# Optimization experiments

Hardware: AMD Instinct MI355X
Metric: run time of the kernel (lower is better)

Reference implementation:

```python
import jax, jax.numpy as jnp
import numpy as np

SEQ_LEN = 128
EMBED_DIM = 1024
BATCH = 128


def setup_inputs() -> dict:
    key = jax.random.key(0)
    ks = jax.random.split(key, 9)
    d = EMBED_DIM
    s = 0.02
    return {
        "x": jax.random.normal(ks[0], (BATCH, SEQ_LEN * d), dtype=jnp.float32),
        "Wq": jax.random.normal(ks[1], (d, d), dtype=jnp.float32) * s,
        "bq": jax.random.normal(ks[2], (d,), dtype=jnp.float32) * s,
        "Wk": jax.random.normal(ks[3], (d, d), dtype=jnp.float32) * s,
        "bk": jax.random.normal(ks[4], (d,), dtype=jnp.float32) * s,
        "Wv": jax.random.normal(ks[5], (d, d), dtype=jnp.float32) * s,
        "bv": jax.random.normal(ks[6], (d,), dtype=jnp.float32) * s,
        "Wo": jax.random.normal(ks[7], (d, d), dtype=jnp.float32) * s,
        "bo": jax.random.normal(ks[8], (d,), dtype=jnp.float32) * s,
    }


def reference(x, Wq, bq, Wk, bk, Wv, bv, Wo, bo):
    b = x.shape[0]
    d = EMBED_DIM
    xs = x.reshape(b, SEQ_LEN, d)  # [B, S, D]
    # torch Linear: y = x @ W.T + b
    Q = jnp.einsum("bsd,ed->bse", xs, Wq) + bq
    K = jnp.einsum("bsd,ed->bse", xs, Wk) + bk
    V = jnp.einsum("bsd,ed->bse", xs, Wv) + bv
    scores = jnp.einsum("bse,bte->bst", Q, K) / jnp.sqrt(jnp.float32(d))
    weights = jax.nn.softmax(scores, axis=-1)
    attended = jnp.einsum("bst,bte->bse", weights, V)
    out = jnp.einsum("bse,fe->bsf", attended, Wo) + bo
    return out.reshape(b, -1)
```

## Files before the change

### kernel.cpp

```cpp
#include <hip/hip_runtime.h>
#include <hip/hip_bf16.h>

typedef __attribute__((ext_vector_type(8))) __bf16 bf16x8;
typedef __attribute__((ext_vector_type(4))) __bf16 bf16x4;
typedef __attribute__((ext_vector_type(4))) float f32x4;

#define SEQ 128
#define DIM 1024
#define BATCH 128
#define MTOT (BATCH * SEQ)

__device__ __forceinline__ void gload16(const void* g, void* l) {
    __builtin_amdgcn_global_load_lds(
        (const __attribute__((address_space(1))) void*)g,
        (__attribute__((address_space(3))) void*)l, 16, 0, 0);
}

#define BARRIER() do { asm volatile("" ::: "memory"); __builtin_amdgcn_s_barrier(); asm volatile("" ::: "memory"); } while (0)
#define WAITV4() asm volatile("s_waitcnt vmcnt(4)" ::: "memory")
#define WAITV0() asm volatile("s_waitcnt vmcnt(0)" ::: "memory")
#define MFMA(a, b, c) __builtin_amdgcn_mfma_f32_16x16x32_bf16(a, b, c, 0, 0, 0)

__global__ void cast_f32_bf16(const float* __restrict__ in, __bf16* __restrict__ out, int n) {
    int i = (blockIdx.x * blockDim.x + threadIdx.x) * 8;
    if (i >= n) return;
    float4 f0 = *reinterpret_cast<const float4*>(in + i);
    float4 f1 = *reinterpret_cast<const float4*>(in + i + 4);
    bf16x8 o;
    o[0] = (__bf16)f0.x; o[1] = (__bf16)f0.y; o[2] = (__bf16)f0.z; o[3] = (__bf16)f0.w;
    o[4] = (__bf16)f1.x; o[5] = (__bf16)f1.y; o[6] = (__bf16)f1.z; o[7] = (__bf16)f1.w;
    *reinterpret_cast<bf16x8*>(out + i) = o;
}

template <int MODE>
__global__ __launch_bounds__(512, 1) void gemm256(const __bf16* __restrict__ A,
                                                  const __bf16* __restrict__ W,
                                                  const float* __restrict__ bias,
                                                  void* __restrict__ Cout) {
    const int K = 1024, N = 1024;
    __shared__ __bf16 lds[3][4][4096];
    const int tid = threadIdx.x, wave = tid >> 6, lane = tid & 63;
    const int wr = wave >> 2, wc = wave & 3;
    const int lr = lane & 15;
    const int lkb = ((lane >> 4) & 3) * 16;
    const int bid = blockIdx.x;
    const int swz = (bid & 7) * 32 + (bid >> 3);
    const int m0 = (swz >> 2) * 256, n0 = (swz & 3) * 256;
    const int rloc = wave * 16 + (lane >> 2);
    const int cbs  = ((((lane & 3) << 4) ^ (((lane >> 3) & 3) << 4)) >> 1);
    const __bf16* pA = A + (size_t)(m0 + rloc) * K + cbs;
    const __bf16* pB = W + (size_t)(n0 + rloc) * K + cbs;
    const int wo = wave * 512;

    f32x4 acc[8][4] = {};

#define LDF(SLOT, R) (*reinterpret_cast<const bf16x8*>( \
        reinterpret_cast<const char*>(SLOT) + (R) * 64 + (lkb ^ ((((R) >> 1) & 3) << 4))))
#define STAGE_A(SB, TS) do { gload16(pA + (TS) * 32, &lds[SB][0][wo]); \
                             gload16(pA + (size_t)128 * 1024 + (TS) * 32, &lds[SB][1][wo]); } while (0)
#define STAGE_B(SB, TS) do { gload16(pB + (TS) * 32, &lds[SB][2][wo]); \
                             gload16(pB + (size_t)128 * 1024 + (TS) * 32, &lds[SB][3][wo]); } while (0)

#define TILE(RB, SB, TS, DOSTAGE, VMSTMT) do { \
    const __bf16* As_ = &lds[RB][wr][0]; \
    const __bf16* Bs_ = &lds[RB][2 + (wc >> 1)][0]; \
    const int bb_ = (wc & 1) * 64; \
    bf16x8 a0 = LDF(As_, 0 * 16 + lr), a1 = LDF(As_, 1 * 16 + lr); \
    bf16x8 a2 = LDF(As_, 2 * 16 + lr), a3 = LDF(As_, 3 * 16 + lr); \
    bf16x8 b0 = LDF(Bs_, bb_ + 0 * 16 + lr), b1 = LDF(Bs_, bb_ + 1 * 16 + lr); \
    bf16x8 b2 = LDF(Bs_, bb_ + 2 * 16 + lr), b3 = LDF(Bs_, bb_ + 3 * 16 + lr); \
    if (DOSTAGE) STAGE_A(SB, TS); \
    BARRIER(); \
    __builtin_amdgcn_s_setprio(1); \
    acc[0][0] = MFMA(a0, b0, acc[0][0]); acc[0][1] = MFMA(a0, b1, acc[0][1]); \
    acc[0][2] = MFMA(a0, b2, acc[0][2]); acc[0][3] = MFMA(a0, b3, acc[0][3]); \
    acc[1][0] = MFMA(a1, b0, acc[1][0]); acc[1][1] = MFMA(a1, b1, acc[1][1]); \
    acc[1][2] = MFMA(a1, b2, acc[1][2]); acc[1][3] = MFMA(a1, b3, acc[1][3]); \
    acc[2][0] = MFMA(a2, b0, acc[2][0]); acc[2][1] = MFMA(a2, b1, acc[2][1]); \
    acc[2][2] = MFMA(a2, b2, acc[2][2]); acc[2][3] = MFMA(a2, b3, acc[2][3]); \
    acc[3][0] = MFMA(a3, b0, acc[3][0]); acc[3][1] = MFMA(a3, b1, acc[3][1]); \
    acc[3][2] = MFMA(a3, b2, acc[3][2]); acc[3][3] = MFMA(a3, b3, acc[3][3]); \
    __builtin_amdgcn_s_setprio(0); \
    BARRIER(); \
    a0 = LDF(As_, 4 * 16 + lr); a1 = LDF(As_, 5 * 16 + lr); \
    a2 = LDF(As_, 6 * 16 + lr); a3 = LDF(As_, 7 * 16 + lr); \
    if (DOSTAGE) STAGE_B(SB, TS); \
    BARRIER(); \
    __builtin_amdgcn_s_setprio(1); \
    acc[4][0] = MFMA(a0, b0, acc[4][0]); acc[4][1] = MFMA(a0, b1, acc[4][1]); \
    acc[4][2] = MFMA(a0, b2, acc[4][2]); acc[4][3] = MFMA(a0, b3, acc[4][3]); \
    acc[5][0] = MFMA(a1, b0, acc[5][0]); acc[5][1] = MFMA(a1, b1, acc[5][1]); \
    acc[5][2] = MFMA(a1, b2, acc[5][2]); acc[5][3] = MFMA(a1, b3, acc[5][3]); \
    acc[6][0] = MFMA(a2, b0, acc[6][0]); acc[6][1] = MFMA(a2, b1, acc[6][1]); \
    acc[6][2] = MFMA(a2, b2, acc[6][2]); acc[6][3] = MFMA(a2, b3, acc[6][3]); \
    acc[7][0] = MFMA(a3, b0, acc[7][0]); acc[7][1] = MFMA(a3, b1, acc[7][1]); \
    acc[7][2] = MFMA(a3, b2, acc[7][2]); acc[7][3] = MFMA(a3, b3, acc[7][3]); \
    __builtin_amdgcn_s_setprio(0); \
    VMSTMT; \
    BARRIER(); \
} while (0)

    STAGE_A(0, 0); STAGE_B(0, 0);
    STAGE_A(1, 1); STAGE_B(1, 1);
    WAITV4();
    BARRIER();

    for (int it = 0; it < 10; ++it) {
        const int t = it * 3;
        TILE(0, 2, t + 2, 1, WAITV4());
        TILE(1, 0, t + 3, 1, WAITV4());
        TILE(2, 1, t + 4, 1, WAITV4());
    }
    TILE(0, 0, 0, 0, WAITV0());
    TILE(1, 0, 0, 0, (void)0);

    const int rbase = (lane >> 4) * 4;
    #pragma unroll
    for (int ri = 0; ri < 8; ++ri) {
        #pragma unroll
        for (int j = 0; j < 4; ++j) {
            const int gc  = n0 + wc * 64 + j * 16 + lr;
            const float bv = bias[gc];
            const int grb = m0 + wr * 128 + ri * 16 + rbase;
            if (MODE == 0) {
                __bf16* C = (__bf16*)Cout;
                #pragma unroll
                for (int r = 0; r < 4; ++r)
                    C[(size_t)(grb + r) * N + gc] = (__bf16)(acc[ri][j][r] + bv);
            } else if (MODE == 1) {
                float* C = (float*)Cout;
                #pragma unroll
                for (int r = 0; r < 4; ++r)
                    C[(size_t)(grb + r) * N + gc] = acc[ri][j][r] + bv;
            } else {
                __bf16* C = (__bf16*)Cout;
                const int b = grb >> 7, s = grb & 127;
                bf16x4 v;
                #pragma unroll
                for (int r = 0; r < 4; ++r) v[r] = (__bf16)(acc[ri][j][r] + bv);
                *reinterpret_cast<bf16x4*>(&C[((size_t)b * DIM + gc) * SEQ + s]) = v;
            }
        }
    }
#undef TILE
#undef STAGE_A
#undef STAGE_B
#undef LDF
}

__global__ __launch_bounds__(256) void attn_kernel(const __bf16* __restrict__ Q,
                                                   const __bf16* __restrict__ Km,
                                                   const __bf16* __restrict__ Vt,
                                                   __bf16* __restrict__ Ab) {
    __shared__ float  Ssh[32][132];
    __shared__ __bf16 Psh[32][136];
    const int bid = blockIdx.x;
    const int logical = (bid & 7) * 64 + (bid >> 3);
    const int b = logical >> 2, rt = logical & 3;
    const int tid = threadIdx.x, wave = tid >> 6, lane = tid & 63;
    const int lr = lane & 15, lk = (lane >> 4) * 8, rbase = (lane >> 4) * 4;
    const __bf16* Qb = Q  + ((size_t)b * SEQ + rt * 32) * DIM;
    const __bf16* Kb = Km + (size_t)b * SEQ * DIM;
    const __bf16* Vb = Vt + (size_t)b * DIM * SEQ;

    f32x4 acc[2][2] = {};
    for (int k0 = 0; k0 < DIM; k0 += 32) {
        bf16x8 qf[2], kf[2];
        #pragma unroll
        for (int i = 0; i < 2; ++i)
            qf[i] = *reinterpret_cast<const bf16x8*>(&Qb[(size_t)(i * 16 + lr) * DIM + k0 + lk]);
        #pragma unroll
        for (int j = 0; j < 2; ++j)
            kf[j] = *reinterpret_cast<const bf16x8*>(&Kb[(size_t)(wave * 32 + j * 16 + lr) * DIM + k0 + lk]);
        #pragma unroll
        for (int i = 0; i < 2; ++i)
            #pragma unroll
            for (int j = 0; j < 2; ++j)
                acc[i][j] = MFMA(qf[i], kf[j], acc[i][j]);
    }
    const float scale = 0.03125f;
    #pragma unroll
    for (int i = 0; i < 2; ++i)
        #pragma unroll
        for (int j = 0; j < 2; ++j)
            #pragma unroll
            for (int r = 0; r < 4; ++r)
                Ssh[i * 16 + rbase + r][wave * 32 + j * 16 + lr] = acc[i][j][r] * scale;
    __syncthreads();

    {
        const int row = tid >> 3;
        const int c0  = (tid & 7) * 16;
        float4 v0 = *reinterpret_cast<const float4*>(&Ssh[row][c0]);
        float4 v1 = *reinterpret_cast<const float4*>(&Ssh[row][c0 + 4]);
        float4 v2 = *reinterpret_cast<const float4*>(&Ssh[row][c0 + 8]);
        float4 v3 = *reinterpret_cast<const float4*>(&Ssh[row][c0 + 12]);
        float e[16] = {v0.x, v0.y, v0.z, v0.w, v1.x, v1.y, v1.z, v1.w,
                       v2.x, v2.y, v2.z, v2.w, v3.x, v3.y, v3.z, v3.w};
        float mx = e[0];
        #pragma unroll
        for (int u = 1; u < 16; ++u) mx = fmaxf(mx, e[u]);
        mx = fmaxf(mx, __shfl_xor(mx, 1));
        mx = fmaxf(mx, __shfl_xor(mx, 2));
        mx = fmaxf(mx, __shfl_xor(mx, 4));
        float s = 0.f;
        #pragma unroll
        for (int u = 0; u < 16; ++u) { e[u] = __expf(e[u] - mx); s += e[u]; }
        s += __shfl_xor(s, 1);
        s += __shfl_xor(s, 2);
        s += __shfl_xor(s, 4);
        const float inv = 1.f / s;
        bf16x8 p0, p1;
        #pragma unroll
        for (int u = 0; u < 8; ++u) { p0[u] = (__bf16)(e[u] * inv); p1[u] = (__bf16)(e[u + 8] * inv); }
        *reinterpret_cast<bf16x8*>(&Psh[row][c0])     = p0;
        *reinterpret_cast<bf16x8*>(&Psh[row][c0 + 8]) = p1;
    }
    __syncthreads();

    bf16x8 pf[2][4];
    #pragma unroll
    for (int i = 0; i < 2; ++i)
        #pragma unroll
        for (int ks = 0; ks < 4; ++ks)
            pf[i][ks] = *reinterpret_cast<const bf16x8*>(&Psh[i * 16 + lr][ks * 32 + lk]);
    __bf16* Ao = Ab + ((size_t)b * SEQ + rt * 32) * DIM;
    for (int n0 = wave * 256; n0 < wave * 256 + 256; n0 += 16) {
        f32x4 a2[2] = {};
        #pragma unroll
        for (int ks = 0; ks < 4; ++ks) {
            bf16x8 vf = *reinterpret_cast<const bf16x8*>(&Vb[(size_t)(n0 + lr) * SEQ + ks * 32 + lk]);
            #pragma unroll
            for (int i = 0; i < 2; ++i)
                a2[i] = MFMA(pf[i][ks], vf, a2[i]);
        }
        #pragma unroll
        for (int i = 0; i < 2; ++i)
            #pragma unroll
            for (int r = 0; r < 4; ++r)
                Ao[(size_t)(i * 16 + rbase + r) * DIM + n0 + lr] = (__bf16)a2[i][r];
    }
}

extern "C" void kernel_launch(void* const* d_in, const int* in_sizes, int n_in,
                              void* d_out, int out_size, void* d_ws, size_t ws_size,
                              hipStream_t stream) {
    const float* x  = (const float*)d_in[0];
    const float* Wq = (const float*)d_in[1];
    const float* bq = (const float*)d_in[2];
    const float* Wk = (const float*)d_in[3];
    const float* bk = (const float*)d_in[4];
    const float* Wv = (const float*)d_in[5];
    const float* bv = (const float*)d_in[6];
    const float* Wo = (const float*)d_in[7];
    const float* bo = (const float*)d_in[8];

    char* ws = (char*)d_ws;
    const size_t MB = 1024 * 1024;
    __bf16* Xb  = (__bf16*)(ws);
    __bf16* Wqb = (__bf16*)(ws + 32 * MB);
    __bf16* Wkb = (__bf16*)(ws + 34 * MB);
    __bf16* Wvb = (__bf16*)(ws + 36 * MB);
    __bf16* Wob = (__bf16*)(ws + 38 * MB);
    __bf16* Qb  = (__bf16*)(ws + 40 * MB);
    __bf16* Kb  = (__bf16*)(ws + 72 * MB);
    __bf16* Vt  = (__bf16*)(ws + 104 * MB);
    __bf16* Ab  = Xb;

    const int nX = MTOT * DIM;
    const int nW = DIM * DIM;
    cast_f32_bf16<<<nX / 8 / 256, 256, 0, stream>>>(x, Xb, nX);
    cast_f32_bf16<<<nW / 8 / 256, 256, 0, stream>>>(Wq, Wqb, nW);
    cast_f32_bf16<<<nW / 8 / 256, 256, 0, stream>>>(Wk, Wkb, nW);
    cast_f32_bf16<<<nW / 8 / 256, 256, 0, stream>>>(Wv, Wvb, nW);
    cast_f32_bf16<<<nW / 8 / 256, 256, 0, stream>>>(Wo, Wob, nW);

    gemm256<0><<<256, 512, 0, stream>>>(Xb, Wqb, bq, (void*)Qb);
    gemm256<0><<<256, 512, 0, stream>>>(Xb, Wkb, bk, (void*)Kb);
    gemm256<2><<<256, 512, 0, stream>>>(Xb, Wvb, bv, (void*)Vt);

    attn_kernel<<<512, 256, 0, stream>>>(Qb, Kb, Vt, Ab);

    gemm256<1><<<256, 512, 0, stream>>>(Ab, Wob, bo, d_out);
}
```

Baseline: 225.0 us.

## Stage attention K/Q and V tiles through swizzled double-buffered LDS

Replaces the direct per-lane global loads of Q, K and V in the attention kernel with cooperative global_load_lds staging into an XOR-swizzled, double-buffered shared-memory region. The next chunk is prefetched while MFMAs run on the current one. The goal is to cut uncoalesced global traffic and load latency in the QK^T and PV phases. In exchange it adds barriers, a larger 40 KB LDS footprint that can reduce occupancy, and hand-tuned vmcnt waits. Those waits must line up exactly with the number of interleaved global stores still outstanding.

```diff
diff --git a/kernel.cpp b/kernel.cpp
--- a/kernel.cpp
+++ b/kernel.cpp
@@ -17,8 +17,7 @@
 }
 
 #define BARRIER() do { asm volatile("" ::: "memory"); __builtin_amdgcn_s_barrier(); asm volatile("" ::: "memory"); } while (0)
-#define WAITV4() asm volatile("s_waitcnt vmcnt(4)" ::: "memory")
-#define WAITV0() asm volatile("s_waitcnt vmcnt(0)" ::: "memory")
+#define WAITV(N) asm volatile("s_waitcnt vmcnt(" #N ")" ::: "memory")
 #define MFMA(a, b, c) __builtin_amdgcn_mfma_f32_16x16x32_bf16(a, b, c, 0, 0, 0)
 
 __global__ void cast_f32_bf16(const float* __restrict__ in, __bf16* __restrict__ out, int n) {
@@ -102,16 +101,16 @@
 
     STAGE_A(0, 0); STAGE_B(0, 0);
     STAGE_A(1, 1); STAGE_B(1, 1);
-    WAITV4();
+    WAITV(4);
     BARRIER();
 
     for (int it = 0; it < 10; ++it) {
         const int t = it * 3;
-        TILE(0, 2, t + 2, 1, WAITV4());
-        TILE(1, 0, t + 3, 1, WAITV4());
-        TILE(2, 1, t + 4, 1, WAITV4());
-    }
-    TILE(0, 0, 0, 0, WAITV0());
+        TILE(0, 2, t + 2, 1, WAITV(4));
+        TILE(1, 0, t + 3, 1, WAITV(4));
+        TILE(2, 1, t + 4, 1, WAITV(4));
+    }
+    TILE(0, 0, 0, 0, WAITV(0));
     TILE(1, 0, 0, 0, (void)0);
 
     const int rbase = (lane >> 4) * 4;
@@ -152,8 +151,10 @@
                                                    const __bf16* __restrict__ Km,
                                                    const __bf16* __restrict__ Vt,
                                                    __bf16* __restrict__ Ab) {
-    __shared__ float  Ssh[32][132];
-    __shared__ __bf16 Psh[32][136];
+    __shared__ __align__(16) char smem[40960];
+    float  (*Ssh)[132] = (float(*)[132])(smem);
+    __bf16 (*Psh)[136] = (__bf16(*)[136])(smem + 16896);
+
     const int bid = blockIdx.x;
     const int logical = (bid & 7) * 64 + (bid >> 3);
     const int b = logical >> 2, rt = logical & 3;
@@ -163,20 +164,57 @@
     const __bf16* Kb = Km + (size_t)b * SEQ * DIM;
     const __bf16* Vb = Vt + (size_t)b * DIM * SEQ;
 
+    const int csrc = ((lane & 7) * 16) ^ (((lane >> 3) & 7) << 4);
+
     f32x4 acc[2][2] = {};
-    for (int k0 = 0; k0 < DIM; k0 += 32) {
-        bf16x8 qf[2], kf[2];
-        #pragma unroll
-        for (int i = 0; i < 2; ++i)
-            qf[i] = *reinterpret_cast<const bf16x8*>(&Qb[(size_t)(i * 16 + lr) * DIM + k0 + lk]);
-        #pragma unroll
-        for (int j = 0; j < 2; ++j)
-            kf[j] = *reinterpret_cast<const bf16x8*>(&Kb[(size_t)(wave * 32 + j * 16 + lr) * DIM + k0 + lk]);
-        #pragma unroll
-        for (int i = 0; i < 2; ++i)
+    {
+        auto stage_kq = [&](int buf, int c) {
+            char* Kd = smem + buf * 20480 + wave * 4096;
+            char* Qd = smem + buf * 20480 + 16384 + wave * 1024;
+            const char* Ks = (const char*)Kb + (size_t)(wave * 32 + (lane >> 3)) * 2048 + c * 128 + csrc;
+            #pragma unroll
+            for (int q = 0; q < 4; ++q)
+                gload16(Ks + (size_t)q * 8 * 2048, Kd + q * 1024);
+            const char* Qs = (const char*)Qb + (size_t)(wave * 8 + (lane >> 3)) * 2048 + c * 128 + csrc;
+            gload16(Qs, Qd);
+        };
+        stage_kq(0, 0);
+        WAITV(0);
+        BARRIER();
+        for (int c = 0; c < 16; ++c) {
+            const int rb = c & 1;
+            if (c < 15) stage_kq(rb ^ 1, c + 1);
+            const char* Kl = smem + rb * 20480;
+            const char* Ql = Kl + 16384;
+            bf16x8 qf[2][2], kf[2][2];
+            #pragma unroll
+            for (int i = 0; i < 2; ++i)
+                #pragma unroll
+                for (int ks = 0; ks < 2; ++ks) {
+                    const int r = i * 16 + lr;
+                    qf[i][ks] = *reinterpret_cast<const bf16x8*>(
+                        Ql + r * 128 + ((ks * 64 + (lane >> 4) * 16) ^ ((r & 7) << 4)));
+                }
             #pragma unroll
             for (int j = 0; j < 2; ++j)
-                acc[i][j] = MFMA(qf[i], kf[j], acc[i][j]);
+                #pragma unroll
+                for (int ks = 0; ks < 2; ++ks) {
+                    const int r = wave * 32 + j * 16 + lr;
+                    kf[j][ks] = *reinterpret_cast<const bf16x8*>(
+                        Kl + r * 128 + ((ks * 64 + (lane >> 4) * 16) ^ ((r & 7) << 4)));
+                }
+            __builtin_amdgcn_s_setprio(1);
+            #pragma unroll
+            for (int i = 0; i < 2; ++i)
+                #pragma unroll
+                for (int j = 0; j < 2; ++j)
+                    #pragma unroll
+                    for (int ks = 0; ks < 2; ++ks)
+                        acc[i][j] = MFMA(qf[i][ks], kf[j][ks], acc[i][j]);
+            __builtin_amdgcn_s_setprio(0);
+            WAITV(0);
+            BARRIER();
+        }
     }
     const float scale = 0.03125f;
     #pragma unroll
@@ -224,21 +262,45 @@
         #pragma unroll
         for (int ks = 0; ks < 4; ++ks)
             pf[i][ks] = *reinterpret_cast<const bf16x8*>(&Psh[i * 16 + lr][ks * 32 + lk]);
+    __syncthreads();
+
     __bf16* Ao = Ab + ((size_t)b * SEQ + rt * 32) * DIM;
-    for (int n0 = wave * 256; n0 < wave * 256 + 256; n0 += 16) {
-        f32x4 a2[2] = {};
-        #pragma unroll
-        for (int ks = 0; ks < 4; ++ks) {
-            bf16x8 vf = *reinterpret_cast<const bf16x8*>(&Vb[(size_t)(n0 + lr) * SEQ + ks * 32 + lk]);
+    {
+        auto stage_v = [&](int buf, int c) {
+            char* Vd = smem + buf * 16384 + wave * 4096;
+            #pragma unroll
+            for (int q = 0; q < 4; ++q) {
+                const int rowl = wave * 16 + q * 4 + (lane >> 4);
+                const char* Vs = (const char*)Vb + (size_t)(c * 64 + rowl) * 256 +
+                                 (((lane & 15) * 16) ^ ((rowl & 7) << 4));
+                gload16(Vs, Vd + q * 1024);
+            }
+        };
+        stage_v(0, 0);
+        WAITV(0);
+        BARRIER();
+        for (int c = 0; c < 16; ++c) {
+            const int rb = c & 1;
+            if (c < 15) stage_v(rb ^ 1, c + 1);
+            const char* Vl = smem + rb * 16384;
+            f32x4 a2[2] = {};
+            const int r = wave * 16 + lr;
+            #pragma unroll
+            for (int ks = 0; ks < 4; ++ks) {
+                bf16x8 vf = *reinterpret_cast<const bf16x8*>(
+                    Vl + r * 256 + ((ks * 64 + (lane >> 4) * 16) ^ ((r & 7) << 4)));
+                a2[0] = MFMA(pf[0][ks], vf, a2[0]);
+                a2[1] = MFMA(pf[1][ks], vf, a2[1]);
+            }
+            const int n0 = c * 64 + wave * 16;
             #pragma unroll
             for (int i = 0; i < 2; ++i)
-                a2[i] = MFMA(pf[i][ks], vf, a2[i]);
+                #pragma unroll
+                for (int rr = 0; rr < 4; ++rr)
+                    Ao[(size_t)(i * 16 + rbase + rr) * DIM + n0 + lr] = (__bf16)a2[i][rr];
+            WAITV(8);
+            BARRIER();
         }
-        #pragma unroll
-        for (int i = 0; i < 2; ++i)
-            #pragma unroll
-            for (int r = 0; r < 4; ++r)
-                Ao[(size_t)(i * 16 + rbase + r) * DIM + n0 + lr] = (__bf16)a2[i][r];
     }
 }
 
```

Result: faster. 199.7 us (-11.2%).
